# Optimization experiments

Hardware: AMD Instinct MI355X
Metric: run time of the kernel (lower is better)

Reference implementation:

```python
import jax, jax.numpy as jnp
import numpy as np

BETA_F = 1000.0
BETA_B = 1.0
CLAMP = 12.0
B, C, H, W = 4, 1, 1024, 1024
N_NODES = 262144  # nodes per max-tree


def soft_mask(logits):
    # forward sigmoid with beta_f gain and +-12 clamp (clamp_logits=True)
    return jax.nn.sigmoid(jnp.clip(BETA_F * logits, -CLAMP, CLAMP))


def tree_filter(sigma, levels, parent):
    """Differentiable connected filtering on one max-tree.
    Node value = level(root) + sum over root->node path of sigma_j*(level_j - level_parent_j),
    computed with pointer-doubling ancestor sums (log N gather passes).
    sigma, levels: (N,), parent: (N,) int32 with parent[0]==0 (root).
    """
    N = sigma.shape[0]
    delta = levels - levels[parent]          # per-node gray-level increment
    c = (sigma * delta).at[0].set(levels[0])  # root contributes its level
    # sentinel node N with contribution 0 and self-pointer, terminates chains
    acc = jnp.concatenate([c, jnp.zeros((1,), c.dtype)])
    ptr = jnp.concatenate([parent.at[0].set(N), jnp.full((1,), N, parent.dtype)])
    steps = int(np.ceil(np.log2(N))) + 1
    for _ in range(steps):
        acc, ptr = acc + acc[ptr], ptr[ptr]
    return acc[:N]


def setup_inputs() -> dict:
    rng = np.random.default_rng(0)
    T = B * C  # one tree per (b, c) image
    idx = np.arange(N_NODES)
    # topologically ordered random tree: parent[i] in [0, i), parent[0] = 0
    parent = np.floor(rng.random((T, N_NODES)) * idx).astype(np.int32)
    # monotone increasing gray levels: ancestor-sum of positive increments
    inc = (rng.random((T, N_NODES)) + 0.1).astype(np.float32)
    acc = np.concatenate([inc, np.zeros((T, 1), np.float32)], 1)
    ptr = np.concatenate([parent, np.full((T, 1), N_NODES, np.int64)], 1)
    ptr[:, 0] = N_NODES
    for _ in range(int(np.ceil(np.log2(N_NODES))) + 1):
        acc = acc + np.take_along_axis(acc, ptr, 1)
        ptr = np.take_along_axis(ptr, ptr, 1)
    levels = acc[:, :N_NODES]
    attr_norm = rng.random((T, N_NODES)).astype(np.float32)  # minmax01-normalized attribute
    pixel_to_node = rng.integers(0, N_NODES, (T, H * W)).astype(np.int32)
    x = rng.standard_normal((B, C, H, W)).astype(np.float32)
    return {
        "x": jnp.asarray(x),
        "attr_norm": jnp.asarray(attr_norm),
        "levels": jnp.asarray(levels),
        "thr": jnp.full((1,), 0.5, jnp.float32),  # torch init.constant_(p, 0.5)
        "parent": jnp.asarray(parent),
        "pixel_to_node": jnp.asarray(pixel_to_node),
    }


def reference(x, attr_norm, levels, thr, parent, pixel_to_node):
    # logits = attr_scaled - threshold_norm, per node, per tree
    sigma = soft_mask(attr_norm - thr.reshape(()))          # (T, N)
    v = jax.vmap(tree_filter)(sigma, levels, parent)         # (T, N) filtered node values
    y = jnp.take_along_axis(v, pixel_to_node, axis=1)        # node -> pixel gather
    return y.reshape(B, C, H, W)  # top_hat=False, num_groups=1 -> out_channels=C
```

## Files before the change

### kernel.cpp

```cpp
#include <hip/hip_runtime.h>

#define NT 4
#define NN 262144
#define NMASK (NN - 1)
#define HW 1048576
#define KPRE 8192

#define SWIZ(b, tree, chunk)                \
    int tree  = ((b) & 7) >> 1;             \
    int chunk = (((b) >> 3) << 1) | ((b) & 1);

__global__ __launch_bounds__(256) void k_build(const float* __restrict__ attr,
                                               const float* __restrict__ levels,
                                               const float* __restrict__ thr,
                                               const int* __restrict__ parent,
                                               int2* __restrict__ cmb,
                                               float* __restrict__ v) {
    __shared__ float lvcs[KPRE];
    __shared__ unsigned short ps[KPRE];

    int b = blockIdx.x;
    if (b < 32) {
        int tree = (b & 7) >> 1;
        int sub  = ((b >> 3) << 1) | (b & 1);
        int tbase = tree << 18;
        float t0 = thr[0];

        for (int j = threadIdx.x; j < KPRE; j += 256) {
            lvcs[j] = levels[tbase + j];
            ps[j] = (unsigned short)(parent[tbase + j] & (KPRE - 1));
        }
        __syncthreads();

        float creg[32];
#pragma unroll
        for (int k = 0; k < 32; ++k) {
            int j = threadIdx.x + k * 256;
            float lv = lvcs[j];
            float lp = lvcs[ps[j]];
            float z = 1000.0f * (attr[tbase + j] - t0);
            z = fminf(fmaxf(z, -12.0f), 12.0f);
            float s = 1.0f / (1.0f + __expf(-z));
            creg[k] = (j == 0) ? lv : s * (lv - lp);
        }
        __syncthreads();
#pragma unroll
        for (int k = 0; k < 32; ++k) lvcs[threadIdx.x + k * 256] = creg[k];
        __syncthreads();

        int   cur[4];
        float acc[4];
        int alive = 0xF;
#pragma unroll
        for (int k = 0; k < 4; ++k) { cur[k] = sub * 1024 + threadIdx.x + k * 256; acc[k] = 0.0f; }
        for (int it = 0; it < 64 && __any(alive); ++it) {
#pragma unroll
            for (int k = 0; k < 4; ++k) {
                if (alive & (1 << k)) {
                    int c_ = cur[k];
                    acc[k] += lvcs[c_];
                    if (c_ == 0) alive &= ~(1 << k);
                    else cur[k] = ps[c_];
                }
            }
        }
#pragma unroll
        for (int k = 0; k < 4; ++k)
            v[tbase + sub * 1024 + threadIdx.x + k * 256] = acc[k];
        return;
    }

    int g = b - 32;
    SWIZ(g, tree, chunk0)
    int chunk = 8 + chunk0;
    int tbase = tree << 18;
    int idx4 = chunk * 256 + threadIdx.x;
    int4   p4 = ((const int4*)(parent + tbase))[idx4];
    float4 a4 = ((const float4*)(attr + tbase))[idx4];
    float4 l4 = ((const float4*)(levels + tbase))[idx4];
    float t0 = thr[0];

    int   pe[4] = {p4.x & NMASK, p4.y & NMASK, p4.z & NMASK, p4.w & NMASK};
    float ae[4] = {a4.x, a4.y, a4.z, a4.w};
    float le[4] = {l4.x, l4.y, l4.z, l4.w};
    int   oc[8];
#pragma unroll
    for (int e = 0; e < 4; ++e) {
        float lp = levels[tbase + pe[e]];
        float z = 1000.0f * (ae[e] - t0);
        z = fminf(fmaxf(z, -12.0f), 12.0f);
        float s = 1.0f / (1.0f + __expf(-z));
        oc[2 * e] = pe[e];
        oc[2 * e + 1] = __float_as_int(s * (le[e] - lp));
    }
    int4* dst = (int4*)(cmb + tbase);
    dst[2 * idx4]     = make_int4(oc[0], oc[1], oc[2], oc[3]);
    dst[2 * idx4 + 1] = make_int4(oc[4], oc[5], oc[6], oc[7]);
}

__global__ __launch_bounds__(256) void k_walk(const int2* __restrict__ cmb,
                                              float* __restrict__ v) {
    SWIZ(blockIdx.x, tree, chunk)
    int base = KPRE + chunk * 1024;
    const int2*  ct = cmb + (tree << 18);
    const float* vt = v + (tree << 18);

    int   cur[4];
    float acc[4];
    int alive = 0xF;
#pragma unroll
    for (int k = 0; k < 4; ++k) { cur[k] = base + threadIdx.x + k * 256; acc[k] = 0.0f; }

    for (int it = 0; it < 64 && __any(alive); ++it) {
#pragma unroll
        for (int k = 0; k < 4; ++k) {
            if (alive & (1 << k)) {
                int2 rec = ct[cur[k]];
                acc[k] += __int_as_float(rec.y);
                int nxt = rec.x;
                if (nxt < KPRE) {
                    acc[k] += vt[nxt];
                    alive &= ~(1 << k);
                } else {
                    cur[k] = nxt;
                }
            }
        }
    }
#pragma unroll
    for (int k = 0; k < 4; ++k)
        v[(tree << 18) + base + threadIdx.x + k * 256] = acc[k];
}

__global__ __launch_bounds__(256) void k_pix(const float* __restrict__ v,
                                             const int* __restrict__ p2n,
                                             float* __restrict__ y) {
    SWIZ(blockIdx.x, tree, chunk)
    int i4 = (tree << 18) + chunk * 256 + threadIdx.x;
    int4 idx = ((const int4*)p2n)[i4];
    const float* vt = v + (tree << 18);
    float4 o;
    o.x = vt[idx.x & NMASK];
    o.y = vt[idx.y & NMASK];
    o.z = vt[idx.z & NMASK];
    o.w = vt[idx.w & NMASK];
    ((float4*)y)[i4] = o;
}

extern "C" void kernel_launch(void* const* d_in, const int* in_sizes, int n_in,
                              void* d_out, int out_size, void* d_ws, size_t ws_size,
                              hipStream_t stream) {
    const float* attr   = (const float*)d_in[1];
    const float* levels = (const float*)d_in[2];
    const float* thr    = (const float*)d_in[3];
    const int*   parent = (const int*)d_in[4];
    const int*   p2n    = (const int*)d_in[5];
    float*       y      = (float*)d_out;

    int2*  cmb = (int2*)d_ws;
    float* v   = (float*)((char*)d_ws + (size_t)NT * NN * 8);

    k_build<<<32 + NT * (NN - KPRE) / 1024, 256, 0, stream>>>(attr, levels, thr, parent, cmb, v);
    k_walk <<<NT * (NN - KPRE) / 1024, 256, 0, stream>>>(cmb, v);
    k_pix  <<<NT * HW / 1024, 256, 0, stream>>>(v, p2n, y);
}
```

Measured before the change: 142.0 us.

## Split prefix-tree walk into separate kernel and use nontemporal loads/stores

Moves the first-8192-node shared-memory ancestor walk out of k_build into its own k_prefix kernel with one 1024-thread block per tree. This removes the 32 heavy blocks that shared a launch with the streaming build blocks. It also switches the streamed reads of parent, attr and pixel_to_node, and the output writes, to nontemporal loads and stores to reduce cache pollution. The cost is one extra launch, and the prefix work becomes serialized on only 4 blocks instead of 32.

Result: slower. 153.0 us (+7.8%).

```diff
diff --git a/kernel.cpp b/kernel.cpp
--- a/kernel.cpp
+++ b/kernel.cpp
@@ -6,96 +6,94 @@
 #define HW 1048576
 #define KPRE 8192
 
+typedef int   vi4 __attribute__((ext_vector_type(4)));
+typedef float vf4 __attribute__((ext_vector_type(4)));
+
 #define SWIZ(b, tree, chunk)                \
     int tree  = ((b) & 7) >> 1;             \
     int chunk = (((b) >> 3) << 1) | ((b) & 1);
+
+__global__ __launch_bounds__(1024) void k_prefix(const float* __restrict__ attr,
+                                                 const float* __restrict__ levels,
+                                                 const float* __restrict__ thr,
+                                                 const int* __restrict__ parent,
+                                                 float* __restrict__ v) {
+    __shared__ float lvcs[KPRE];
+    __shared__ unsigned short ps[KPRE];
+    int tree = blockIdx.x;
+    int tbase = tree << 18;
+    float t0 = thr[0];
+
+    for (int j = threadIdx.x; j < KPRE; j += 1024) {
+        lvcs[j] = levels[tbase + j];
+        ps[j] = (unsigned short)(parent[tbase + j] & (KPRE - 1));
+    }
+    __syncthreads();
+
+    float creg[8];
+#pragma unroll
+    for (int k = 0; k < 8; ++k) {
+        int j = threadIdx.x + k * 1024;
+        float lv = lvcs[j];
+        float lp = lvcs[ps[j]];
+        float z = 1000.0f * (attr[tbase + j] - t0);
+        z = fminf(fmaxf(z, -12.0f), 12.0f);
+        float s = 1.0f / (1.0f + __expf(-z));
+        creg[k] = (j == 0) ? lv : s * (lv - lp);
+    }
+    __syncthreads();
+#pragma unroll
+    for (int k = 0; k < 8; ++k) lvcs[threadIdx.x + k * 1024] = creg[k];
+    __syncthreads();
+
+    int   cur[8];
+    float acc[8];
+    int alive = 0xFF;
+#pragma unroll
+    for (int k = 0; k < 8; ++k) { cur[k] = threadIdx.x + k * 1024; acc[k] = 0.0f; }
+    for (int it = 0; it < 64 && __any(alive); ++it) {
+#pragma unroll
+        for (int k = 0; k < 8; ++k) {
+            if (alive & (1 << k)) {
+                int c_ = cur[k];
+                acc[k] += lvcs[c_];
+                if (c_ == 0) alive &= ~(1 << k);
+                else cur[k] = ps[c_];
+            }
+        }
+    }
+#pragma unroll
+    for (int k = 0; k < 8; ++k)
+        v[tbase + threadIdx.x + k * 1024] = acc[k];
+}
 
 __global__ __launch_bounds__(256) void k_build(const float* __restrict__ attr,
                                                const float* __restrict__ levels,
                                                const float* __restrict__ thr,
                                                const int* __restrict__ parent,
-                                               int2* __restrict__ cmb,
-                                               float* __restrict__ v) {
-    __shared__ float lvcs[KPRE];
-    __shared__ unsigned short ps[KPRE];
-
-    int b = blockIdx.x;
-    if (b < 32) {
-        int tree = (b & 7) >> 1;
-        int sub  = ((b >> 3) << 1) | (b & 1);
-        int tbase = tree << 18;
-        float t0 = thr[0];
-
-        for (int j = threadIdx.x; j < KPRE; j += 256) {
-            lvcs[j] = levels[tbase + j];
-            ps[j] = (unsigned short)(parent[tbase + j] & (KPRE - 1));
-        }
-        __syncthreads();
-
-        float creg[32];
-#pragma unroll
-        for (int k = 0; k < 32; ++k) {
-            int j = threadIdx.x + k * 256;
-            float lv = lvcs[j];
-            float lp = lvcs[ps[j]];
-            float z = 1000.0f * (attr[tbase + j] - t0);
-            z = fminf(fmaxf(z, -12.0f), 12.0f);
-            float s = 1.0f / (1.0f + __expf(-z));
-            creg[k] = (j == 0) ? lv : s * (lv - lp);
-        }
-        __syncthreads();
-#pragma unroll
-        for (int k = 0; k < 32; ++k) lvcs[threadIdx.x + k * 256] = creg[k];
-        __syncthreads();
-
-        int   cur[4];
-        float acc[4];
-        int alive = 0xF;
-#pragma unroll
-        for (int k = 0; k < 4; ++k) { cur[k] = sub * 1024 + threadIdx.x + k * 256; acc[k] = 0.0f; }
-        for (int it = 0; it < 64 && __any(alive); ++it) {
-#pragma unroll
-            for (int k = 0; k < 4; ++k) {
-                if (alive & (1 << k)) {
-                    int c_ = cur[k];
-                    acc[k] += lvcs[c_];
-                    if (c_ == 0) alive &= ~(1 << k);
-                    else cur[k] = ps[c_];
-                }
-            }
-        }
-#pragma unroll
-        for (int k = 0; k < 4; ++k)
-            v[tbase + sub * 1024 + threadIdx.x + k * 256] = acc[k];
-        return;
-    }
-
-    int g = b - 32;
-    SWIZ(g, tree, chunk0)
-    int chunk = 8 + chunk0;
+                                               int2* __restrict__ cmb) {
+    SWIZ(blockIdx.x, tree, chunk)
     int tbase = tree << 18;
-    int idx4 = chunk * 256 + threadIdx.x;
-    int4   p4 = ((const int4*)(parent + tbase))[idx4];
-    float4 a4 = ((const float4*)(attr + tbase))[idx4];
-    float4 l4 = ((const float4*)(levels + tbase))[idx4];
+    int idx4 = KPRE / 4 + chunk * 256 + threadIdx.x;
+    vi4 p4 = __builtin_nontemporal_load(&((const vi4*)(parent + tbase))[idx4]);
+    vf4 a4 = __builtin_nontemporal_load(&((const vf4*)(attr + tbase))[idx4]);
+    vf4 l4 = ((const vf4*)(levels + tbase))[idx4];
     float t0 = thr[0];
 
-    int   pe[4] = {p4.x & NMASK, p4.y & NMASK, p4.z & NMASK, p4.w & NMASK};
-    float ae[4] = {a4.x, a4.y, a4.z, a4.w};
-    float le[4] = {l4.x, l4.y, l4.z, l4.w};
     int   oc[8];
 #pragma unroll
     for (int e = 0; e < 4; ++e) {
-        float lp = levels[tbase + pe[e]];
-        float z = 1000.0f * (ae[e] - t0);
+        int p = p4[e] & NMASK;
+        float lp = levels[tbase + p];
+        float z = 1000.0f * (a4[e] - t0);
         z = fminf(fmaxf(z, -12.0f), 12.0f);
         float s = 1.0f / (1.0f + __expf(-z));
-        oc[2 * e] = pe[e];
-        oc[2 * e + 1] = __float_as_int(s * (le[e] - lp));
+        oc[2 * e] = p;
+        oc[2 * e + 1] = __float_as_int(s * (l4[e] - lp));
     }
-    int4* dst = (int4*)(cmb + tbase);
-    dst[2 * idx4]     = make_int4(oc[0], oc[1], oc[2], oc[3]);
-    dst[2 * idx4 + 1] = make_int4(oc[4], oc[5], oc[6], oc[7]);
+    vi4* dst = (vi4*)(cmb + tbase);
+    dst[2 * idx4]     = (vi4){oc[0], oc[1], oc[2], oc[3]};
+    dst[2 * idx4 + 1] = (vi4){oc[4], oc[5], oc[6], oc[7]};
 }
 
 __global__ __launch_bounds__(256) void k_walk(const int2* __restrict__ cmb,
@@ -137,14 +135,14 @@
                                              float* __restrict__ y) {
     SWIZ(blockIdx.x, tree, chunk)
     int i4 = (tree << 18) + chunk * 256 + threadIdx.x;
-    int4 idx = ((const int4*)p2n)[i4];
+    vi4 idx = __builtin_nontemporal_load(&((const vi4*)p2n)[i4]);
     const float* vt = v + (tree << 18);
-    float4 o;
+    vf4 o;
     o.x = vt[idx.x & NMASK];
     o.y = vt[idx.y & NMASK];
     o.z = vt[idx.z & NMASK];
     o.w = vt[idx.w & NMASK];
-    ((float4*)y)[i4] = o;
+    __builtin_nontemporal_store(o, &((vf4*)y)[i4]);
 }
 
 extern "C" void kernel_launch(void* const* d_in, const int* in_sizes, int n_in,
@@ -160,7 +158,8 @@
     int2*  cmb = (int2*)d_ws;
     float* v   = (float*)((char*)d_ws + (size_t)NT * NN * 8);
 
-    k_build<<<32 + NT * (NN - KPRE) / 1024, 256, 0, stream>>>(attr, levels, thr, parent, cmb, v);
-    k_walk <<<NT * (NN - KPRE) / 1024, 256, 0, stream>>>(cmb, v);
-    k_pix  <<<NT * HW / 1024, 256, 0, stream>>>(v, p2n, y);
+    k_prefix<<<NT, 1024, 0, stream>>>(attr, levels, thr, parent, v);
+    k_build <<<NT * (NN - KPRE) / 1024, 256, 0, stream>>>(attr, levels, thr, parent, cmb);
+    k_walk  <<<NT * (NN - KPRE) / 1024, 256, 0, stream>>>(cmb, v);
+    k_pix   <<<NT * HW / 1024, 256, 0, stream>>>(v, p2n, y);
 }
```
